# Kernel tuning notes

Hardware: AMD Instinct MI355X
Metric: run time of the kernel (lower is better)

The kernel has to match this reference:

```python
import jax, jax.numpy as jnp
import numpy as np

N_NODES, N_EDGES, CH, FEAT = 20000, 320000, 256, 118


def setup_inputs() -> dict:
    key = jax.random.key(0)
    ks = jax.random.split(key, 8)
    x = jax.random.uniform(ks[0], (N_NODES, FEAT), dtype=jnp.float32)
    edge_index = jax.random.randint(ks[1], (2, N_EDGES), 0, N_NODES, dtype=jnp.int64)
    s = 0.05
    W_embed = jax.random.normal(ks[2], (FEAT, CH), dtype=jnp.float32) * s
    b_embed = jnp.zeros((CH,), jnp.float32)
    W1 = jax.random.normal(ks[3], (CH, CH), dtype=jnp.float32) * s
    b1 = jnp.zeros((CH,), jnp.float32)
    W2 = jax.random.normal(ks[4], (CH, CH), dtype=jnp.float32) * s
    b2 = jnp.zeros((CH,), jnp.float32)
    return {"x": x, "edge_index": edge_index, "W_embed": W_embed, "b_embed": b_embed,
            "W1": W1, "b1": b1, "W2": W2, "b2": b2}


def reference(x, edge_index, W_embed, b_embed, W1, b1, W2, b2):
    n = x.shape[0]
    # node embedding: Linear(118 -> C)
    h = x @ W_embed + b_embed  # [N, C]
    src, dst = edge_index[0], edge_index[1]
    # message: gather x_j per edge, dense1 + exact GELU (dropout = identity in eval)
    msg = jax.nn.gelu(h[src] @ W1 + b1, approximate=False)  # [E, C]
    # mean aggregation into destination nodes
    agg = jax.ops.segment_sum(msg, dst, num_segments=n)  # [N, C]
    cnt = jax.ops.segment_sum(jnp.ones((msg.shape[0],), msg.dtype), dst, num_segments=n)
    agg = agg / jnp.maximum(cnt, 1.0)[:, None]
    # update: dense2 + exact GELU
    out = jax.nn.gelu(agg @ W2 + b2, approximate=False)  # [N, C]
    # final mean over channel dim
    return out.mean(axis=1)  # [N]
```

## Files before the change

### kernel.cpp

```cpp
#include <hip/hip_runtime.h>
#include <math.h>

#define N_NODES 20000
#define N_EDGES 320000
#define CH      256
#define FEAT    118
#define CAP     48

typedef float    f32x4 __attribute__((ext_vector_type(4)));
typedef short    s16x8 __attribute__((ext_vector_type(8)));
typedef _Float16 f16x4 __attribute__((ext_vector_type(4)));
typedef _Float16 f16x8 __attribute__((ext_vector_type(8)));
typedef unsigned short u16;

union Frag  { s16x8 v; u16 u[8]; };
union FragH { f16x8 v; _Float16 h[8]; };

__device__ __forceinline__ float gelu_exact(float x) {
    return 0.5f * x * (1.0f + erff(x * 0.70710678118654752f));
}
__device__ __forceinline__ u16 f2bf(float f) {
    unsigned u = __float_as_uint(f);
    u = (u + 0x7FFFu + ((u >> 16) & 1u)) >> 16;
    return (u16)u;
}
__device__ __forceinline__ float bf2f(u16 h) { return __uint_as_float(((unsigned)h) << 16); }

__global__ __launch_bounds__(256) void prep0(const float* __restrict__ We,
                                             const float* __restrict__ be,
                                             const float* __restrict__ W1,
                                             const float* __restrict__ b1,
                                             const float* __restrict__ W2,
                                             _Float16* __restrict__ w2h, _Float16* __restrict__ w2l,
                                             u16* __restrict__ wch, u16* __restrict__ wcl,
                                             float* __restrict__ bc,
                                             int* __restrict__ cnt) {
    const int b = blockIdx.x, tid = threadIdx.x;
    if (b < 32) {
        int fid = b * 256 + tid;
        int lane = fid & 63, ks = (fid >> 6) & 7, nt = fid >> 9;
        int n = nt * 16 + (lane & 15);
        int k0 = ks * 32 + (lane >> 4) * 8;
        FragH hi, lo;
        #pragma unroll
        for (int j = 0; j < 8; j++) {
            float v = W2[(size_t)(k0 + j) * 256 + n];
            _Float16 h = (_Float16)v;
            hi.h[j] = h;
            lo.h[j] = (_Float16)((v - (float)h) * 4096.0f);
        }
        ((f16x8*)w2h)[fid] = hi.v;
        ((f16x8*)w2l)[fid] = lo.v;
    } else if (b < 161) {
        int f = b - 32;
        int n = tid;
        if (f < 128) {
            float acc = 0.0f;
            if (f < FEAT) {
                const float* wr = We + (size_t)f * 256;
                #pragma unroll 8
                for (int c = 0; c < 256; c++) acc += wr[c] * W1[(size_t)c * 256 + n];
            }
            int nt = n >> 4, lm = n & 15, ks = f >> 5, q = (f >> 3) & 3, j = f & 7;
            size_t idx = (((size_t)nt * 4 + ks) * 64 + q * 16 + lm) * 8 + j;
            u16 h = f2bf(acc);
            wch[idx] = h;
            wcl[idx] = f2bf(acc - bf2f(h));
        } else {
            float acc = b1[n];
            #pragma unroll 8
            for (int c = 0; c < 256; c++) acc += be[c] * W1[(size_t)c * 256 + n];
            bc[n] = acc;
        }
    } else {
        int idx = (b - 161) * 256 + tid;
        if (idx < N_NODES) cnt[idx] = 0;
    }
}

__global__ __launch_bounds__(256) void main_fused(const float* __restrict__ x,
                                                  const int* __restrict__ ei,
                                                  const u16* __restrict__ Bh_, const u16* __restrict__ Bl_,
                                                  const float* __restrict__ bias,
                                                  int* __restrict__ cnt, int* __restrict__ bins,
                                                  _Float16* __restrict__ Mout) {
    if (blockIdx.x >= 1250) {
        int e = (blockIdx.x - 1250) * 256 + threadIdx.x;
        int s = ei[e];
        int d = ei[N_EDGES + e];
        int p = atomicAdd(&cnt[d], 1);
        if (p < CAP) bins[(size_t)d * CAP + p] = s;
        return;
    }
    __shared__ float xs[16][132];
    __shared__ _Float16 Ls[16][256];
    const int tid = threadIdx.x, wave = tid >> 6, lane = tid & 63;
    const int quad = lane >> 4, lm = lane & 15;
    const int mt = blockIdx.x, nt0 = wave * 4;
    {
        int r = tid >> 4, ci = tid & 15;
        const float* xrow = x + (size_t)(mt * 16 + r) * FEAT;
        #pragma unroll
        for (int it = 0; it < 8; it++) {
            int col = ci + it * 16;
            xs[r][col] = (col < FEAT) ? xrow[col] : 0.0f;
        }
    }
    __syncthreads();
    s16x8 a_h[4], a_l[4];
    #pragma unroll
    for (int ks = 0; ks < 4; ks++) {
        int k0 = ks * 32 + quad * 8;
        Frag hi, lo;
        #pragma unroll
        for (int j = 0; j < 8; j++) {
            float v = xs[lm][k0 + j];
            u16 h = f2bf(v);
            hi.u[j] = h; lo.u[j] = f2bf(v - bf2f(h));
        }
        a_h[ks] = hi.v; a_l[ks] = lo.v;
    }
    const s16x8* Bh = (const s16x8*)Bh_; const s16x8* Bl = (const s16x8*)Bl_;
    f32x4 acc[4] = {f32x4{0,0,0,0}, f32x4{0,0,0,0}, f32x4{0,0,0,0}, f32x4{0,0,0,0}};
    #pragma unroll
    for (int ks = 0; ks < 4; ks++) {
        #pragma unroll
        for (int t = 0; t < 4; t++) {
            s16x8 bh = Bh[((size_t)(nt0 + t) * 4 + ks) * 64 + lane];
            s16x8 bl = Bl[((size_t)(nt0 + t) * 4 + ks) * 64 + lane];
            acc[t] = __builtin_amdgcn_mfma_f32_16x16x32_bf16(a_h[ks], bh, acc[t], 0, 0, 0);
            acc[t] = __builtin_amdgcn_mfma_f32_16x16x32_bf16(a_l[ks], bh, acc[t], 0, 0, 0);
            acc[t] = __builtin_amdgcn_mfma_f32_16x16x32_bf16(a_h[ks], bl, acc[t], 0, 0, 0);
        }
    }
    #pragma unroll
    for (int t = 0; t < 4; t++) {
        float bn = bias[(nt0 + t) * 16 + lm];
        #pragma unroll
        for (int r = 0; r < 4; r++)
            Ls[quad * 4 + r][(nt0 + t) * 16 + lm] = (_Float16)gelu_exact(acc[t][r] + bn);
    }
    __syncthreads();
    s16x8* dst = (s16x8*)Mout + (size_t)mt * 512;
    const s16x8* src = (const s16x8*)&Ls[0][0];
    dst[tid]       = src[tid];
    dst[256 + tid] = src[256 + tid];
}

__global__ __launch_bounds__(256) void aggmean(const _Float16* __restrict__ M,
                                               const int* __restrict__ cnt,
                                               const int* __restrict__ bins,
                                               const _Float16* __restrict__ Bh_,
                                               const _Float16* __restrict__ Bl_,
                                               const float* __restrict__ bias,
                                               float* __restrict__ out) {
    __shared__ f16x8 af[8][64];
    __shared__ float part[4][16];
    const int tid = threadIdx.x, wave = tid >> 6, lane = tid & 63;
    const int half = lane >> 5, lh = lane & 31;
    const int node0 = blockIdx.x * 16;
    for (int ni = 0; ni < 4; ni++) {
        int node = node0 + wave * 4 + ni;
        int c = cnt[node];
        int cc = min(c, CAP);
        int myid = (lane < cc) ? bins[(size_t)node * CAP + lane] : 0;
        float a[8] = {0.f, 0.f, 0.f, 0.f, 0.f, 0.f, 0.f, 0.f};
        for (int j = 0; j < cc; j += 8) {
            f16x8 v[4];
            #pragma unroll
            for (int u = 0; u < 4; u++) {
                int e = min(j + u * 2 + half, cc - 1);
                int s = __shfl(myid, e, 64);
                v[u] = *(const f16x8*)(M + (size_t)s * CH + lh * 8);
            }
            #pragma unroll
            for (int u = 0; u < 4; u++) {
                if (j + u * 2 + half < cc) {
                    #pragma unroll
                    for (int q = 0; q < 8; q++) a[q] += (float)v[u][q];
                }
            }
        }
        #pragma unroll
        for (int q = 0; q < 8; q++) a[q] += __shfl_xor(a[q], 32, 64);
        if (half == 0) {
            float inv = 1.0f / (float)max(c, 1);
            FragH o;
            #pragma unroll
            for (int q = 0; q < 8; q++) o.h[q] = (_Float16)(a[q] * inv);
            af[lh >> 2][(lh & 3) * 16 + (wave * 4 + ni)] = o.v;
        }
    }
    __syncthreads();
    const int quad = lane >> 4, lm = lane & 15;
    const int nt0 = wave * 4;
    const f16x8* Bh = (const f16x8*)Bh_;
    const f16x8* Bl = (const f16x8*)Bl_;
    f32x4 acch[4] = {f32x4{0,0,0,0}, f32x4{0,0,0,0}, f32x4{0,0,0,0}, f32x4{0,0,0,0}};
    f32x4 accl[4] = {f32x4{0,0,0,0}, f32x4{0,0,0,0}, f32x4{0,0,0,0}, f32x4{0,0,0,0}};
    #pragma unroll
    for (int ks = 0; ks < 8; ks++) {
        f16x8 a = af[ks][lane];
        #pragma unroll
        for (int t = 0; t < 4; t++) {
            f16x8 bh = Bh[((size_t)(nt0 + t) * 8 + ks) * 64 + lane];
            f16x8 bl = Bl[((size_t)(nt0 + t) * 8 + ks) * 64 + lane];
            acch[t] = __builtin_amdgcn_mfma_f32_16x16x32_f16(a, bh, acch[t], 0, 0, 0);
            accl[t] = __builtin_amdgcn_mfma_f32_16x16x32_f16(a, bl, accl[t], 0, 0, 0);
        }
    }
    float p[4] = {0.f, 0.f, 0.f, 0.f};
    #pragma unroll
    for (int t = 0; t < 4; t++) {
        float bn = bias[(nt0 + t) * 16 + lm];
        #pragma unroll
        for (int r = 0; r < 4; r++)
            p[r] += gelu_exact(acch[t][r] + accl[t][r] * (1.0f / 4096.0f) + bn);
    }
    #pragma unroll
    for (int off = 1; off < 16; off <<= 1)
        #pragma unroll
        for (int r = 0; r < 4; r++)
            p[r] += __shfl_xor(p[r], off, 64);
    if (lm == 0)
        #pragma unroll
        for (int r = 0; r < 4; r++)
            part[wave][quad * 4 + r] = p[r];
    __syncthreads();
    if (tid < 16) {
        float s = part[0][tid] + part[1][tid] + part[2][tid] + part[3][tid];
        out[node0 + tid] = s * (1.0f / 256.0f);
    }
}

extern "C" void kernel_launch(void* const* d_in, const int* in_sizes, int n_in,
                              void* d_out, int out_size, void* d_ws, size_t ws_size,
                              hipStream_t stream) {
    const float* x  = (const float*)d_in[0];
    const int*   ei = (const int*)d_in[1];
    const float* We = (const float*)d_in[2];
    const float* be = (const float*)d_in[3];
    const float* W1 = (const float*)d_in[4];
    const float* b1 = (const float*)d_in[5];
    const float* W2 = (const float*)d_in[6];
    const float* b2 = (const float*)d_in[7];
    float* out = (float*)d_out;

    char* ws = (char*)d_ws;
    size_t off = 0;
    _Float16* M = (_Float16*)(ws + off); off += 10240000;
    u16* wch = (u16*)(ws + off); off += 65536;
    u16* wcl = (u16*)(ws + off); off += 65536;
    _Float16* w2h = (_Float16*)(ws + off); off += 131072;
    _Float16* w2l = (_Float16*)(ws + off); off += 131072;
    float* bc = (float*)(ws + off); off += 1024;
    int* cnt  = (int*)(ws + off); off += N_NODES * 4;
    int* bins = (int*)(ws + off); off += (size_t)N_NODES * CAP * 4;

    prep0<<<240, 256, 0, stream>>>(We, be, W1, b1, W2, w2h, w2l, wch, wcl, bc, cnt);
    main_fused<<<2500, 256, 0, stream>>>(x, ei, wch, wcl, bc, cnt, bins, M);
    aggmean<<<N_NODES / 16, 256, 0, stream>>>(M, cnt, bins, w2h, w2l, b2, out);
}
```

Before: 156.4 us.

## Fuse prep, message and aggregation kernels into one cooperative persistent kernel

Merges the weight-prep, message/binning and aggregate+update kernels into a single cooperative kernel of 512 persistent blocks, with grid-wide syncs between phases and a shared-memory union reused across phases. The aggregation phase now handles 32 nodes per block, so each W2 fragment loaded feeds two MFMA row tiles. The aim is to remove the gaps between kernel launches and halve W2 fragment traffic. In exchange it pays for grid barriers, caps occupancy via the persistent grid, and can load-balance poorly when 2500 or 625 work items are strided over 512 blocks.

```diff
diff --git a/kernel.cpp b/kernel.cpp
--- a/kernel.cpp
+++ b/kernel.cpp
@@ -1,5 +1,8 @@
 #include <hip/hip_runtime.h>
+#include <hip/hip_cooperative_groups.h>
 #include <math.h>
+
+namespace cg = cooperative_groups;
 
 #define N_NODES 20000
 #define N_EDGES 320000
@@ -26,210 +29,227 @@
 }
 __device__ __forceinline__ float bf2f(u16 h) { return __uint_as_float(((unsigned)h) << 16); }
 
-__global__ __launch_bounds__(256) void prep0(const float* __restrict__ We,
-                                             const float* __restrict__ be,
-                                             const float* __restrict__ W1,
-                                             const float* __restrict__ b1,
-                                             const float* __restrict__ W2,
-                                             _Float16* __restrict__ w2h, _Float16* __restrict__ w2l,
-                                             u16* __restrict__ wch, u16* __restrict__ wcl,
-                                             float* __restrict__ bc,
-                                             int* __restrict__ cnt) {
-    const int b = blockIdx.x, tid = threadIdx.x;
-    if (b < 32) {
-        int fid = b * 256 + tid;
-        int lane = fid & 63, ks = (fid >> 6) & 7, nt = fid >> 9;
-        int n = nt * 16 + (lane & 15);
-        int k0 = ks * 32 + (lane >> 4) * 8;
-        FragH hi, lo;
-        #pragma unroll
-        for (int j = 0; j < 8; j++) {
-            float v = W2[(size_t)(k0 + j) * 256 + n];
-            _Float16 h = (_Float16)v;
-            hi.h[j] = h;
-            lo.h[j] = (_Float16)((v - (float)h) * 4096.0f);
-        }
-        ((f16x8*)w2h)[fid] = hi.v;
-        ((f16x8*)w2l)[fid] = lo.v;
-    } else if (b < 161) {
-        int f = b - 32;
-        int n = tid;
-        if (f < 128) {
-            float acc = 0.0f;
-            if (f < FEAT) {
-                const float* wr = We + (size_t)f * 256;
-                #pragma unroll 8
-                for (int c = 0; c < 256; c++) acc += wr[c] * W1[(size_t)c * 256 + n];
-            }
-            int nt = n >> 4, lm = n & 15, ks = f >> 5, q = (f >> 3) & 3, j = f & 7;
-            size_t idx = (((size_t)nt * 4 + ks) * 64 + q * 16 + lm) * 8 + j;
-            u16 h = f2bf(acc);
-            wch[idx] = h;
-            wcl[idx] = f2bf(acc - bf2f(h));
-        } else {
-            float acc = b1[n];
-            #pragma unroll 8
-            for (int c = 0; c < 256; c++) acc += be[c] * W1[(size_t)c * 256 + n];
-            bc[n] = acc;
-        }
-    } else {
-        int idx = (b - 161) * 256 + tid;
-        if (idx < N_NODES) cnt[idx] = 0;
-    }
-}
-
-__global__ __launch_bounds__(256) void main_fused(const float* __restrict__ x,
-                                                  const int* __restrict__ ei,
-                                                  const u16* __restrict__ Bh_, const u16* __restrict__ Bl_,
-                                                  const float* __restrict__ bias,
-                                                  int* __restrict__ cnt, int* __restrict__ bins,
-                                                  _Float16* __restrict__ Mout) {
-    if (blockIdx.x >= 1250) {
-        int e = (blockIdx.x - 1250) * 256 + threadIdx.x;
-        int s = ei[e];
-        int d = ei[N_EDGES + e];
-        int p = atomicAdd(&cnt[d], 1);
-        if (p < CAP) bins[(size_t)d * CAP + p] = s;
-        return;
-    }
-    __shared__ float xs[16][132];
-    __shared__ _Float16 Ls[16][256];
+__global__ __launch_bounds__(256, 4) void fused(
+        const float* __restrict__ x,
+        const int* __restrict__ ei,
+        const float* __restrict__ We,
+        const float* __restrict__ be,
+        const float* __restrict__ W1,
+        const float* __restrict__ b1,
+        const float* __restrict__ W2,
+        const float* __restrict__ b2,
+        _Float16* __restrict__ w2h, _Float16* __restrict__ w2l,
+        u16* __restrict__ wch, u16* __restrict__ wcl,
+        float* __restrict__ bc,
+        int* __restrict__ cnt, int* __restrict__ bins,
+        _Float16* __restrict__ M,
+        float* __restrict__ out) {
+    cg::grid_group grid = cg::this_grid();
     const int tid = threadIdx.x, wave = tid >> 6, lane = tid & 63;
     const int quad = lane >> 4, lm = lane & 15;
-    const int mt = blockIdx.x, nt0 = wave * 4;
-    {
-        int r = tid >> 4, ci = tid & 15;
-        const float* xrow = x + (size_t)(mt * 16 + r) * FEAT;
-        #pragma unroll
-        for (int it = 0; it < 8; it++) {
-            int col = ci + it * 16;
-            xs[r][col] = (col < FEAT) ? xrow[col] : 0.0f;
+    const int half = lane >> 5, lh = lane & 31;
+    const int G = gridDim.x;
+
+    __shared__ union {
+        struct { float xs[16][132]; _Float16 Ls[16][256]; } b;
+        struct { f16x8 af[2][8][64]; float part[4][32]; } c;
+    } sm;
+
+    for (int pa = blockIdx.x; pa < 240; pa += G) {
+        if (pa < 32) {
+            int fid = pa * 256 + tid;
+            int ks = (fid >> 6) & 7, nt = fid >> 9;
+            int n = nt * 16 + lm;
+            int k0 = ks * 32 + quad * 8;
+            FragH hi, lo;
+            #pragma unroll
+            for (int j = 0; j < 8; j++) {
+                float v = W2[(size_t)(k0 + j) * 256 + n];
+                _Float16 h = (_Float16)v;
+                hi.h[j] = h;
+                lo.h[j] = (_Float16)((v - (float)h) * 4096.0f);
+            }
+            ((f16x8*)w2h)[fid] = hi.v;
+            ((f16x8*)w2l)[fid] = lo.v;
+        } else if (pa < 161) {
+            int f = pa - 32;
+            int n = tid;
+            if (f < 128) {
+                float acc = 0.0f;
+                if (f < FEAT) {
+                    const float* wr = We + (size_t)f * 256;
+                    #pragma unroll 8
+                    for (int c = 0; c < 256; c++) acc += wr[c] * W1[(size_t)c * 256 + n];
+                }
+                int nt = n >> 4, lmn = n & 15, ks = f >> 5, q = (f >> 3) & 3, j = f & 7;
+                size_t idx = (((size_t)nt * 4 + ks) * 64 + q * 16 + lmn) * 8 + j;
+                u16 h = f2bf(acc);
+                wch[idx] = h;
+                wcl[idx] = f2bf(acc - bf2f(h));
+            } else {
+                float acc = b1[n];
+                #pragma unroll 8
+                for (int c = 0; c < 256; c++) acc += be[c] * W1[(size_t)c * 256 + n];
+                bc[n] = acc;
+            }
+        } else {
+            int idx = (pa - 161) * 256 + tid;
+            if (idx < N_NODES) cnt[idx] = 0;
         }
     }
-    __syncthreads();
-    s16x8 a_h[4], a_l[4];
-    #pragma unroll
-    for (int ks = 0; ks < 4; ks++) {
-        int k0 = ks * 32 + quad * 8;
-        Frag hi, lo;
-        #pragma unroll
-        for (int j = 0; j < 8; j++) {
-            float v = xs[lm][k0 + j];
-            u16 h = f2bf(v);
-            hi.u[j] = h; lo.u[j] = f2bf(v - bf2f(h));
-        }
-        a_h[ks] = hi.v; a_l[ks] = lo.v;
+    grid.sync();
+
+    for (int pb = blockIdx.x; pb < 2500; pb += G) {
+        if (pb >= 1250) {
+            int e = (pb - 1250) * 256 + tid;
+            int s = ei[e];
+            int d = ei[N_EDGES + e];
+            int p = atomicAdd(&cnt[d], 1);
+            if (p < CAP) bins[(size_t)d * CAP + p] = s;
+            continue;
+        }
+        const int mt = pb, nt0 = wave * 4;
+        {
+            int r = tid >> 4, ci = tid & 15;
+            const float* xrow = x + (size_t)(mt * 16 + r) * FEAT;
+            #pragma unroll
+            for (int it = 0; it < 8; it++) {
+                int col = ci + it * 16;
+                sm.b.xs[r][col] = (col < FEAT) ? xrow[col] : 0.0f;
+            }
+        }
+        __syncthreads();
+        s16x8 a_h[4], a_l[4];
+        #pragma unroll
+        for (int ks = 0; ks < 4; ks++) {
+            int k0 = ks * 32 + quad * 8;
+            Frag hi, lo;
+            #pragma unroll
+            for (int j = 0; j < 8; j++) {
+                float v = sm.b.xs[lm][k0 + j];
+                u16 h = f2bf(v);
+                hi.u[j] = h; lo.u[j] = f2bf(v - bf2f(h));
+            }
+            a_h[ks] = hi.v; a_l[ks] = lo.v;
+        }
+        const s16x8* Bh = (const s16x8*)wch; const s16x8* Bl = (const s16x8*)wcl;
+        f32x4 acc[4] = {f32x4{0,0,0,0}, f32x4{0,0,0,0}, f32x4{0,0,0,0}, f32x4{0,0,0,0}};
+        #pragma unroll
+        for (int ks = 0; ks < 4; ks++) {
+            #pragma unroll
+            for (int t = 0; t < 4; t++) {
+                s16x8 bh = Bh[((size_t)(nt0 + t) * 4 + ks) * 64 + lane];
+                s16x8 bl = Bl[((size_t)(nt0 + t) * 4 + ks) * 64 + lane];
+                acc[t] = __builtin_amdgcn_mfma_f32_16x16x32_bf16(a_h[ks], bh, acc[t], 0, 0, 0);
+                acc[t] = __builtin_amdgcn_mfma_f32_16x16x32_bf16(a_l[ks], bh, acc[t], 0, 0, 0);
+                acc[t] = __builtin_amdgcn_mfma_f32_16x16x32_bf16(a_h[ks], bl, acc[t], 0, 0, 0);
+            }
+        }
+        #pragma unroll
+        for (int t = 0; t < 4; t++) {
+            float bn = bc[(nt0 + t) * 16 + lm];
+            #pragma unroll
+            for (int r = 0; r < 4; r++)
+                sm.b.Ls[quad * 4 + r][(nt0 + t) * 16 + lm] = (_Float16)gelu_exact(acc[t][r] + bn);
+        }
+        __syncthreads();
+        s16x8* dst = (s16x8*)M + (size_t)mt * 512;
+        const s16x8* src = (const s16x8*)&sm.b.Ls[0][0];
+        dst[tid]       = src[tid];
+        dst[256 + tid] = src[256 + tid];
     }
-    const s16x8* Bh = (const s16x8*)Bh_; const s16x8* Bl = (const s16x8*)Bl_;
-    f32x4 acc[4] = {f32x4{0,0,0,0}, f32x4{0,0,0,0}, f32x4{0,0,0,0}, f32x4{0,0,0,0}};
-    #pragma unroll
-    for (int ks = 0; ks < 4; ks++) {
+    grid.sync();
+
+    const f16x8* Bh2 = (const f16x8*)w2h;
+    const f16x8* Bl2 = (const f16x8*)w2l;
+    for (int pu = blockIdx.x; pu < 625; pu += G) {
+        const int node0 = pu * 32;
+        for (int ni = 0; ni < 8; ni++) {
+            int rowid = wave * 8 + ni;
+            int node = node0 + rowid;
+            int c = cnt[node];
+            int cc = min(c, CAP);
+            int myid = (lane < cc) ? bins[(size_t)node * CAP + lane] : 0;
+            float a[8] = {0.f, 0.f, 0.f, 0.f, 0.f, 0.f, 0.f, 0.f};
+            for (int j = 0; j < cc; j += 8) {
+                f16x8 v[4];
+                #pragma unroll
+                for (int u = 0; u < 4; u++) {
+                    int e = min(j + u * 2 + half, cc - 1);
+                    int s = __shfl(myid, e, 64);
+                    v[u] = *(const f16x8*)(M + (size_t)s * CH + lh * 8);
+                }
+                #pragma unroll
+                for (int u = 0; u < 4; u++) {
+                    if (j + u * 2 + half < cc) {
+                        #pragma unroll
+                        for (int q = 0; q < 8; q++) a[q] += (float)v[u][q];
+                    }
+                }
+            }
+            #pragma unroll
+            for (int q = 0; q < 8; q++) a[q] += __shfl_xor(a[q], 32, 64);
+            if (half == 0) {
+                float inv = 1.0f / (float)max(c, 1);
+                FragH o;
+                #pragma unroll
+                for (int q = 0; q < 8; q++) o.h[q] = (_Float16)(a[q] * inv);
+                sm.c.af[rowid >> 4][lh >> 2][(lh & 3) * 16 + (rowid & 15)] = o.v;
+            }
+        }
+        __syncthreads();
+        const int nt0 = wave * 4;
+        f32x4 acch[2][4], accl[2][4];
+        #pragma unroll
+        for (int mi = 0; mi < 2; mi++)
+            #pragma unroll
+            for (int t = 0; t < 4; t++) {
+                acch[mi][t] = f32x4{0.f, 0.f, 0.f, 0.f};
+                accl[mi][t] = f32x4{0.f, 0.f, 0.f, 0.f};
+            }
+        #pragma unroll
+        for (int ks = 0; ks < 8; ks++) {
+            f16x8 a0 = sm.c.af[0][ks][lane];
+            f16x8 a1 = sm.c.af[1][ks][lane];
+            #pragma unroll
+            for (int t = 0; t < 4; t++) {
+                f16x8 bh = Bh2[((size_t)(nt0 + t) * 8 + ks) * 64 + lane];
+                f16x8 bl = Bl2[((size_t)(nt0 + t) * 8 + ks) * 64 + lane];
+                acch[0][t] = __builtin_amdgcn_mfma_f32_16x16x32_f16(a0, bh, acch[0][t], 0, 0, 0);
+                accl[0][t] = __builtin_amdgcn_mfma_f32_16x16x32_f16(a0, bl, accl[0][t], 0, 0, 0);
+                acch[1][t] = __builtin_amdgcn_mfma_f32_16x16x32_f16(a1, bh, acch[1][t], 0, 0, 0);
+                accl[1][t] = __builtin_amdgcn_mfma_f32_16x16x32_f16(a1, bl, accl[1][t], 0, 0, 0);
+            }
+        }
+        float p[2][4] = {{0.f,0.f,0.f,0.f},{0.f,0.f,0.f,0.f}};
         #pragma unroll
         for (int t = 0; t < 4; t++) {
-            s16x8 bh = Bh[((size_t)(nt0 + t) * 4 + ks) * 64 + lane];
-            s16x8 bl = Bl[((size_t)(nt0 + t) * 4 + ks) * 64 + lane];
-            acc[t] = __builtin_amdgcn_mfma_f32_16x16x32_bf16(a_h[ks], bh, acc[t], 0, 0, 0);
-            acc[t] = __builtin_amdgcn_mfma_f32_16x16x32_bf16(a_l[ks], bh, acc[t], 0, 0, 0);
-            acc[t] = __builtin_amdgcn_mfma_f32_16x16x32_bf16(a_h[ks], bl, acc[t], 0, 0, 0);
-        }
-    }
-    #pragma unroll
-    for (int t = 0; t < 4; t++) {
-        float bn = bias[(nt0 + t) * 16 + lm];
-        #pragma unroll
-        for (int r = 0; r < 4; r++)
-            Ls[quad * 4 + r][(nt0 + t) * 16 + lm] = (_Float16)gelu_exact(acc[t][r] + bn);
-    }
-    __syncthreads();
-    s16x8* dst = (s16x8*)Mout + (size_t)mt * 512;
-    const s16x8* src = (const s16x8*)&Ls[0][0];
-    dst[tid]       = src[tid];
-    dst[256 + tid] = src[256 + tid];
-}
-
-__global__ __launch_bounds__(256) void aggmean(const _Float16* __restrict__ M,
-                                               const int* __restrict__ cnt,
-                                               const int* __restrict__ bins,
-                                               const _Float16* __restrict__ Bh_,
-                                               const _Float16* __restrict__ Bl_,
-                                               const float* __restrict__ bias,
-                                               float* __restrict__ out) {
-    __shared__ f16x8 af[8][64];
-    __shared__ float part[4][16];
-    const int tid = threadIdx.x, wave = tid >> 6, lane = tid & 63;
-    const int half = lane >> 5, lh = lane & 31;
-    const int node0 = blockIdx.x * 16;
-    for (int ni = 0; ni < 4; ni++) {
-        int node = node0 + wave * 4 + ni;
-        int c = cnt[node];
-        int cc = min(c, CAP);
-        int myid = (lane < cc) ? bins[(size_t)node * CAP + lane] : 0;
-        float a[8] = {0.f, 0.f, 0.f, 0.f, 0.f, 0.f, 0.f, 0.f};
-        for (int j = 0; j < cc; j += 8) {
-            f16x8 v[4];
-            #pragma unroll
-            for (int u = 0; u < 4; u++) {
-                int e = min(j + u * 2 + half, cc - 1);
-                int s = __shfl(myid, e, 64);
-                v[u] = *(const f16x8*)(M + (size_t)s * CH + lh * 8);
-            }
-            #pragma unroll
-            for (int u = 0; u < 4; u++) {
-                if (j + u * 2 + half < cc) {
-                    #pragma unroll
-                    for (int q = 0; q < 8; q++) a[q] += (float)v[u][q];
-                }
-            }
-        }
-        #pragma unroll
-        for (int q = 0; q < 8; q++) a[q] += __shfl_xor(a[q], 32, 64);
-        if (half == 0) {
-            float inv = 1.0f / (float)max(c, 1);
-            FragH o;
-            #pragma unroll
-            for (int q = 0; q < 8; q++) o.h[q] = (_Float16)(a[q] * inv);
-            af[lh >> 2][(lh & 3) * 16 + (wave * 4 + ni)] = o.v;
-        }
-    }
-    __syncthreads();
-    const int quad = lane >> 4, lm = lane & 15;
-    const int nt0 = wave * 4;
-    const f16x8* Bh = (const f16x8*)Bh_;
-    const f16x8* Bl = (const f16x8*)Bl_;
-    f32x4 acch[4] = {f32x4{0,0,0,0}, f32x4{0,0,0,0}, f32x4{0,0,0,0}, f32x4{0,0,0,0}};
-    f32x4 accl[4] = {f32x4{0,0,0,0}, f32x4{0,0,0,0}, f32x4{0,0,0,0}, f32x4{0,0,0,0}};
-    #pragma unroll
-    for (int ks = 0; ks < 8; ks++) {
-        f16x8 a = af[ks][lane];
-        #pragma unroll
-        for (int t = 0; t < 4; t++) {
-            f16x8 bh = Bh[((size_t)(nt0 + t) * 8 + ks) * 64 + lane];
-            f16x8 bl = Bl[((size_t)(nt0 + t) * 8 + ks) * 64 + lane];
-            acch[t] = __builtin_amdgcn_mfma_f32_16x16x32_f16(a, bh, acch[t], 0, 0, 0);
-            accl[t] = __builtin_amdgcn_mfma_f32_16x16x32_f16(a, bl, accl[t], 0, 0, 0);
-        }
-    }
-    float p[4] = {0.f, 0.f, 0.f, 0.f};
-    #pragma unroll
-    for (int t = 0; t < 4; t++) {
-        float bn = bias[(nt0 + t) * 16 + lm];
-        #pragma unroll
-        for (int r = 0; r < 4; r++)
-            p[r] += gelu_exact(acch[t][r] + accl[t][r] * (1.0f / 4096.0f) + bn);
-    }
-    #pragma unroll
-    for (int off = 1; off < 16; off <<= 1)
-        #pragma unroll
-        for (int r = 0; r < 4; r++)
-            p[r] += __shfl_xor(p[r], off, 64);
-    if (lm == 0)
-        #pragma unroll
-        for (int r = 0; r < 4; r++)
-            part[wave][quad * 4 + r] = p[r];
-    __syncthreads();
-    if (tid < 16) {
-        float s = part[0][tid] + part[1][tid] + part[2][tid] + part[3][tid];
-        out[node0 + tid] = s * (1.0f / 256.0f);
+            float bn = b2[(nt0 + t) * 16 + lm];
+            #pragma unroll
+            for (int mi = 0; mi < 2; mi++)
+                #pragma unroll
+                for (int r = 0; r < 4; r++)
+                    p[mi][r] += gelu_exact(acch[mi][t][r] + accl[mi][t][r] * (1.0f / 4096.0f) + bn);
+        }
+        #pragma unroll
+        for (int off = 1; off < 16; off <<= 1)
+            #pragma unroll
+            for (int mi = 0; mi < 2; mi++)
+                #pragma unroll
+                for (int r = 0; r < 4; r++)
+                    p[mi][r] += __shfl_xor(p[mi][r], off, 64);
+        if (lm == 0)
+            #pragma unroll
+            for (int mi = 0; mi < 2; mi++)
+                #pragma unroll
+                for (int r = 0; r < 4; r++)
+                    sm.c.part[wave][mi * 16 + quad * 4 + r] = p[mi][r];
+        __syncthreads();
+        if (tid < 32) {
+            float s = sm.c.part[0][tid] + sm.c.part[1][tid]
+                    + sm.c.part[2][tid] + sm.c.part[3][tid];
+            out[node0 + tid] = s * (1.0f / 256.0f);
+        }
     }
 }
 
@@ -257,7 +277,11 @@
     int* cnt  = (int*)(ws + off); off += N_NODES * 4;
     int* bins = (int*)(ws + off); off += (size_t)N_NODES * CAP * 4;
 
-    prep0<<<240, 256, 0, stream>>>(We, be, W1, b1, W2, w2h, w2l, wch, wcl, bc, cnt);
-    main_fused<<<2500, 256, 0, stream>>>(x, ei, wch, wcl, bc, cnt, bins, M);
-    aggmean<<<N_NODES / 16, 256, 0, stream>>>(M, cnt, bins, w2h, w2l, b2, out);
-}
+    void* args[] = { (void*)&x, (void*)&ei, (void*)&We, (void*)&be,
+                     (void*)&W1, (void*)&b1, (void*)&W2, (void*)&b2,
+                     (void*)&w2h, (void*)&w2l, (void*)&wch, (void*)&wcl,
+                     (void*)&bc, (void*)&cnt, (void*)&bins, (void*)&M,
+                     (void*)&out };
+    hipLaunchCooperativeKernel((const void*)fused, dim3(512), dim3(256),
+                               args, 0, stream);
+}
```

After: 315.9 us. +102.0%, slower.
